# Performance work log

Hardware: AMD Instinct MI355X
Metric: run time of the kernel (lower is better)

## Reference

```python
import jax, jax.numpy as jnp
import numpy as np

N, P, D = 262144, 128, 64
EPS = 1e-5
NEG = -1e30


def setup_inputs() -> dict:
    key = jax.random.key(0)
    ks = jax.random.split(key, 12)
    feature = jax.random.normal(ks[0], (N, D), jnp.float32)
    feature_geo = jax.random.normal(ks[1], (N, D), jnp.float32)
    xyz = jax.random.uniform(ks[2], (N, 3), jnp.float32)
    centers = jax.random.uniform(ks[3], (3,), jnp.float32)
    plane_center = jax.random.uniform(ks[4], (P, 3), jnp.float32)
    nrm = jax.random.normal(ks[5], (P, 3), jnp.float32)
    plane_normal = nrm / jnp.linalg.norm(nrm, axis=1, keepdims=True)
    lo = 0.3 * jax.random.uniform(ks[6], (P, 3), jnp.float32)
    hi = 0.5 + 0.5 * jax.random.uniform(ks[7], (P, 3), jnp.float32)
    # exactly two active axes per plane (one axis of the aabb is zeroed)
    ax = jnp.arange(P) % 3
    keep = (jnp.arange(3)[None, :] != ax[:, None]).astype(jnp.float32)
    plane_xyz_min = lo * keep
    plane_xyz_max = hi * keep
    w1 = 0.05 * jax.random.normal(ks[8], (2 * D, D), jnp.float32)
    b1 = jnp.zeros((D,), jnp.float32)
    w2 = 0.05 * jax.random.normal(ks[9], (D, D), jnp.float32)
    b2 = jnp.zeros((D,), jnp.float32)
    w3 = 0.05 * jax.random.normal(ks[10], (D, 1), jnp.float32)
    b3 = jnp.zeros((1,), jnp.float32)
    g1 = jnp.ones((D,), jnp.float32); be1 = jnp.zeros((D,), jnp.float32)
    m1 = jnp.zeros((D,), jnp.float32); v1 = jnp.ones((D,), jnp.float32)
    g2 = jnp.ones((D,), jnp.float32); be2 = jnp.zeros((D,), jnp.float32)
    m2 = jnp.zeros((D,), jnp.float32); v2 = jnp.ones((D,), jnp.float32)
    return dict(feature=feature, feature_geo=feature_geo, xyz=xyz, centers=centers,
                plane_center=plane_center, plane_normal=plane_normal,
                plane_xyz_min=plane_xyz_min, plane_xyz_max=plane_xyz_max,
                w1=w1, b1=b1, g1=g1, be1=be1, m1=m1, v1=v1,
                w2=w2, b2=b2, g2=g2, be2=be2, m2=m2, v2=v2,
                w3=w3, b3=b3)


def _bn(x, g, b, m, v):
    return (x - m) * (g * jax.lax.rsqrt(v + EPS)) + b


def reference(feature, feature_geo, xyz, centers, plane_center, plane_normal,
              plane_xyz_min, plane_xyz_max, w1, b1, g1, be1, m1, v1,
              w2, b2, g2, be2, m2, v2, w3, b3):
    clouds = xyz + centers                                   # [N,3]
    f = jnp.concatenate([feature, feature_geo], axis=1)      # [N,2D]
    # 1x1 conv MLP == per-point matmul (fc1 -> fc2 with BN+ReLU, fc3)
    h1 = jax.nn.relu(_bn(f @ w1 + b1, g1, be1, m1, v1))      # [N,D]
    h2 = jax.nn.relu(_bn(h1 @ w2 + b2, g2, be2, m2, v2))     # [N,D]
    scores = jax.nn.relu(h2 @ w3 + b3)[:, 0]                 # [N]
    # per-plane aabb mask over the two active axes (xyz_max != 0)
    active = plane_xyz_max != 0                              # [P,3]
    in_rng = (clouds[None] >= plane_xyz_min[:, None]) & (clouds[None] < plane_xyz_max[:, None])
    range_mask = jnp.all(in_rng | ~active[:, None, :], axis=-1)   # [P,N]
    # point-to-plane distance: |(clouds - center) . normal|
    dots = clouds @ plane_normal.T                           # [N,P]
    offs = jnp.sum(plane_center * plane_normal, axis=1)      # [P]
    dist = jnp.abs(dots - offs[None, :]).T                   # [P,N]
    mask = range_mask & (dist < 0.1)                         # [P,N]
    sig = jax.nn.sigmoid(scores)                             # [N]
    on_mask = mask & (sig > 0.5)[None, :]
    off_mask = mask & (sig <= 0.5)[None, :]

    def pool(m):  # masked max-pool of fc2 features over points of one plane
        val = jnp.max(jnp.where(m[:, None], h2, NEG), axis=0)     # [D]
        return jnp.where(jnp.any(m), val, 0.0)

    on_feat = jax.lax.map(pool, on_mask)                     # [P,D]
    off_feat = jax.lax.map(pool, off_mask)                   # [P,D]
    scores_masked = jnp.where(mask, scores[None, :], 0.0)    # [P,N]
    return scores_masked, mask, on_mask, off_mask, on_feat, off_feat
```

## Files before the change

### kernel.cpp

```cpp
#include <hip/hip_runtime.h>
#include <hip/hip_bf16.h>
#include <math.h>

#define NPTS 262144
#define NP   128
#define DD   64
#define NWORDS (NPTS / 64)

#define AS4 __attribute__((address_space(4)))
typedef float evf4 __attribute__((ext_vector_type(4)));
typedef AS4 const float* csf;
typedef AS4 const evf4*  csf4;
#define TO_CSF(p)  ((csf)(unsigned long long)(const void*)(p))
#define TO_CSF4(p) ((csf4)(unsigned long long)(const void*)(p))

__global__ __launch_bounds__(256) void prep_kernel(
    const float* __restrict__ plane_center, const float* __restrict__ plane_normal,
    const float* __restrict__ pmin, const float* __restrict__ pmax,
    const float* __restrict__ w2,
    float* __restrict__ packed, float* __restrict__ w2T,
    float* __restrict__ out_feats)
{
    const int t = threadIdx.x;
    out_feats[blockIdx.x * 256 + t] = 0.0f;
    if (blockIdx.x == 0 && t < NP) {
        float n0 = plane_normal[t*3+0], n1 = plane_normal[t*3+1], n2 = plane_normal[t*3+2];
        float c0 = plane_center[t*3+0], c1 = plane_center[t*3+1], c2 = plane_center[t*3+2];
        float off = (c0*n0 + c1*n1) + c2*n2;
        float4* pp = reinterpret_cast<float4*>(packed) + t * 3;
        pp[0] = make_float4(n0, n1, n2, off);
        pp[1] = make_float4(pmin[t*3+0], pmin[t*3+1], pmin[t*3+2], 0.0f);
        pp[2] = make_float4(pmax[t*3+0], pmax[t*3+1], pmax[t*3+2], 0.0f);
    }
    if (blockIdx.x == 1) {
#pragma unroll
        for (int u = 0; u < 16; ++u) {
            const int e = u * 256 + t;
            const int j = e >> 6, k = e & 63;
            w2T[e] = w2[k * DD + j];
        }
    }
}

__global__ __launch_bounds__(256) void fused_kernel(
    const float* __restrict__ feature, const float* __restrict__ feature_geo,
    const float* __restrict__ xyz, const float* __restrict__ centers,
    const float* __restrict__ packed,
    const float* __restrict__ w1, const float* __restrict__ b1,
    const float* __restrict__ g1, const float* __restrict__ be1,
    const float* __restrict__ m1, const float* __restrict__ v1,
    const float* __restrict__ w2T, const float* __restrict__ b2,
    const float* __restrict__ g2, const float* __restrict__ be2,
    const float* __restrict__ m2, const float* __restrict__ v2,
    const float* __restrict__ w3, const float* __restrict__ b3,
    float* __restrict__ h2_out,
    float* __restrict__ out_sm, float* __restrict__ out_mask,
    float* __restrict__ out_on, float* __restrict__ out_off,
    unsigned long long* __restrict__ hitOn, unsigned long long* __restrict__ hitOff)
{
    __shared__ float sw1[128 * DD];
    __shared__ float sw2[DD * DD];
    const int t = threadIdx.x;
    const int n = blockIdx.x * 256 + t;
    const int lane = t & 63;
    const int word = n >> 6;

    {
        const float4* s1 = reinterpret_cast<const float4*>(w1);
        const float4* s2 = reinterpret_cast<const float4*>(w2T);
        float4* d1 = reinterpret_cast<float4*>(sw1);
        float4* d2 = reinterpret_cast<float4*>(sw2);
#pragma unroll
        for (int k = 0; k < 8; ++k) d1[t + k * 256] = s1[t + k * 256];
#pragma unroll
        for (int k = 0; k < 4; ++k) d2[t + k * 256] = s2[t + k * 256];
    }

    const csf cc = TO_CSF(centers);
    const float c0 = xyz[n*3+0] + cc[0];
    const float c1 = xyz[n*3+1] + cc[1];
    const float c2 = xyz[n*3+2] + cc[2];

    __syncthreads();

    float acc[DD];
#pragma unroll
    for (int j = 0; j < DD; ++j) acc[j] = 0.0f;

    const float4* fA = reinterpret_cast<const float4*>(feature) + (size_t)n * 16;
    const float4* fB = reinterpret_cast<const float4*>(feature_geo) + (size_t)n * 16;
#pragma unroll 1
    for (int q = 0; q < 16; ++q) {
        const float4 fv = fA[q];
        const evf4* wr = reinterpret_cast<const evf4*>(sw1 + q * 4 * DD);
#pragma unroll
        for (int j4 = 0; j4 < 16; ++j4) { const evf4 w = wr[j4];
            acc[4*j4+0] = fmaf(fv.x, w.x, acc[4*j4+0]);
            acc[4*j4+1] = fmaf(fv.x, w.y, acc[4*j4+1]);
            acc[4*j4+2] = fmaf(fv.x, w.z, acc[4*j4+2]);
            acc[4*j4+3] = fmaf(fv.x, w.w, acc[4*j4+3]); }
#pragma unroll
        for (int j4 = 0; j4 < 16; ++j4) { const evf4 w = wr[16 + j4];
            acc[4*j4+0] = fmaf(fv.y, w.x, acc[4*j4+0]);
            acc[4*j4+1] = fmaf(fv.y, w.y, acc[4*j4+1]);
            acc[4*j4+2] = fmaf(fv.y, w.z, acc[4*j4+2]);
            acc[4*j4+3] = fmaf(fv.y, w.w, acc[4*j4+3]); }
#pragma unroll
        for (int j4 = 0; j4 < 16; ++j4) { const evf4 w = wr[32 + j4];
            acc[4*j4+0] = fmaf(fv.z, w.x, acc[4*j4+0]);
            acc[4*j4+1] = fmaf(fv.z, w.y, acc[4*j4+1]);
            acc[4*j4+2] = fmaf(fv.z, w.z, acc[4*j4+2]);
            acc[4*j4+3] = fmaf(fv.z, w.w, acc[4*j4+3]); }
#pragma unroll
        for (int j4 = 0; j4 < 16; ++j4) { const evf4 w = wr[48 + j4];
            acc[4*j4+0] = fmaf(fv.w, w.x, acc[4*j4+0]);
            acc[4*j4+1] = fmaf(fv.w, w.y, acc[4*j4+1]);
            acc[4*j4+2] = fmaf(fv.w, w.z, acc[4*j4+2]);
            acc[4*j4+3] = fmaf(fv.w, w.w, acc[4*j4+3]); }
    }
#pragma unroll 1
    for (int q = 0; q < 16; ++q) {
        const float4 fv = fB[q];
        const evf4* wr = reinterpret_cast<const evf4*>(sw1 + (DD + q * 4) * DD);
#pragma unroll
        for (int j4 = 0; j4 < 16; ++j4) { const evf4 w = wr[j4];
            acc[4*j4+0] = fmaf(fv.x, w.x, acc[4*j4+0]);
            acc[4*j4+1] = fmaf(fv.x, w.y, acc[4*j4+1]);
            acc[4*j4+2] = fmaf(fv.x, w.z, acc[4*j4+2]);
            acc[4*j4+3] = fmaf(fv.x, w.w, acc[4*j4+3]); }
#pragma unroll
        for (int j4 = 0; j4 < 16; ++j4) { const evf4 w = wr[16 + j4];
            acc[4*j4+0] = fmaf(fv.y, w.x, acc[4*j4+0]);
            acc[4*j4+1] = fmaf(fv.y, w.y, acc[4*j4+1]);
            acc[4*j4+2] = fmaf(fv.y, w.z, acc[4*j4+2]);
            acc[4*j4+3] = fmaf(fv.y, w.w, acc[4*j4+3]); }
#pragma unroll
        for (int j4 = 0; j4 < 16; ++j4) { const evf4 w = wr[32 + j4];
            acc[4*j4+0] = fmaf(fv.z, w.x, acc[4*j4+0]);
            acc[4*j4+1] = fmaf(fv.z, w.y, acc[4*j4+1]);
            acc[4*j4+2] = fmaf(fv.z, w.z, acc[4*j4+2]);
            acc[4*j4+3] = fmaf(fv.z, w.w, acc[4*j4+3]); }
#pragma unroll
        for (int j4 = 0; j4 < 16; ++j4) { const evf4 w = wr[48 + j4];
            acc[4*j4+0] = fmaf(fv.w, w.x, acc[4*j4+0]);
            acc[4*j4+1] = fmaf(fv.w, w.y, acc[4*j4+1]);
            acc[4*j4+2] = fmaf(fv.w, w.z, acc[4*j4+2]);
            acc[4*j4+3] = fmaf(fv.w, w.w, acc[4*j4+3]); }
    }
    {
        const csf g1c = TO_CSF(g1), v1c = TO_CSF(v1), b1c = TO_CSF(b1),
                  m1c = TO_CSF(m1), be1c = TO_CSF(be1);
#pragma unroll
        for (int j = 0; j < DD; ++j) {
            float sc = g1c[j] * (1.0f / sqrtf(v1c[j] + 1e-5f));
            float h  = fmaf(acc[j] + b1c[j] - m1c[j], sc, be1c[j]);
            acc[j] = fmaxf(h, 0.0f);
        }
    }

    const csf g2c = TO_CSF(g2), v2c = TO_CSF(v2), b2c = TO_CSF(b2),
              m2c = TO_CSF(m2), be2c = TO_CSF(be2), w3c = TO_CSF(w3);
    float s = 0.0f;
    float4* o = reinterpret_cast<float4*>(h2_out) + (size_t)n * 16;
#pragma unroll 1
    for (int jq = 0; jq < 16; ++jq) {
        const evf4* r0 = reinterpret_cast<const evf4*>(sw2 + (4*jq + 0) * DD);
        const evf4* r1 = reinterpret_cast<const evf4*>(sw2 + (4*jq + 1) * DD);
        const evf4* r2 = reinterpret_cast<const evf4*>(sw2 + (4*jq + 2) * DD);
        const evf4* r3 = reinterpret_cast<const evf4*>(sw2 + (4*jq + 3) * DD);
        float a0 = 0.0f, a1 = 0.0f, a2 = 0.0f, a3 = 0.0f;
#pragma unroll
        for (int k4 = 0; k4 < 16; ++k4) {
            const evf4 w0 = r0[k4], w1v = r1[k4], w2v = r2[k4], w3v = r3[k4];
            const float h0 = acc[4*k4+0], h1v = acc[4*k4+1],
                        h2v = acc[4*k4+2], h3v = acc[4*k4+3];
            a0 = fmaf(h0, w0.x, a0); a0 = fmaf(h1v, w0.y, a0);
            a0 = fmaf(h2v, w0.z, a0); a0 = fmaf(h3v, w0.w, a0);
            a1 = fmaf(h0, w1v.x, a1); a1 = fmaf(h1v, w1v.y, a1);
            a1 = fmaf(h2v, w1v.z, a1); a1 = fmaf(h3v, w1v.w, a1);
            a2 = fmaf(h0, w2v.x, a2); a2 = fmaf(h1v, w2v.y, a2);
            a2 = fmaf(h2v, w2v.z, a2); a2 = fmaf(h3v, w2v.w, a2);
            a3 = fmaf(h0, w3v.x, a3); a3 = fmaf(h1v, w3v.y, a3);
            a3 = fmaf(h2v, w3v.z, a3); a3 = fmaf(h3v, w3v.w, a3);
        }
        float hv[4] = {a0, a1, a2, a3};
#pragma unroll
        for (int u = 0; u < 4; ++u) {
            const int jj = 4*jq + u;
            float sc = g2c[jj] * (1.0f / sqrtf(v2c[jj] + 1e-5f));
            float h  = fmaf(hv[u] + b2c[jj] - m2c[jj], sc, be2c[jj]);
            h = fmaxf(h, 0.0f);
            hv[u] = h;
            s = fmaf(h, w3c[jj], s);
        }
        o[jq] = make_float4(hv[0], hv[1], hv[2], hv[3]);
    }
    s += TO_CSF(b3)[0];
    const float score = fmaxf(s, 0.0f);

    const bool on = (0.5f + 0.5f * tanhf(0.5f * score)) > 0.5f;

    const csf4 pp = TO_CSF4(packed);
#pragma unroll 1
    for (int p = 0; p < NP; ++p) {
        const evf4 nrm = pp[p*3+0];
        const evf4 mn  = pp[p*3+1];
        const evf4 mx  = pp[p*3+2];
        float d = fabsf(fmaf(c2, nrm.z, fmaf(c1, nrm.y, c0 * nrm.x)) - nrm.w);
        bool ok0 = (mx.x == 0.0f) | ((c0 >= mn.x) & (c0 < mx.x));
        bool ok1 = (mx.y == 0.0f) | ((c1 >= mn.y) & (c1 < mx.y));
        bool ok2 = (mx.z == 0.0f) | ((c2 >= mn.z) & (c2 < mx.z));
        bool mk  = ok0 & ok1 & ok2 & (d < 0.1f);
        const size_t idx = (size_t)p * NPTS + n;
        const bool mon  = mk & on;
        const bool moff = mk & (!on);
        out_mask[idx] = mk ? 1.0f : 0.0f;
        out_sm[idx]   = mk ? score : 0.0f;
        out_on[idx]   = mon ? 1.0f : 0.0f;
        out_off[idx]  = moff ? 1.0f : 0.0f;
        unsigned long long bOn  = __ballot(mon);
        unsigned long long bOff = __ballot(moff);
        if (lane == 0) {
            hitOn [(size_t)p * NWORDS + word] = bOn;
            hitOff[(size_t)p * NWORDS + word] = bOff;
        }
    }
}

__global__ __launch_bounds__(256) void pool_kernel(
    const float* __restrict__ h2,
    const unsigned long long* __restrict__ hitOn,
    const unsigned long long* __restrict__ hitOff,
    int* __restrict__ out_feats_i)
{
    __shared__ float tile[128 * DD];
    __shared__ unsigned long long bm[2][NP][2];
    const int t = threadIdx.x;
    const int lane = t & 63;
    const int wv = t >> 6;

    float accOn[32], accOff[32];
#pragma unroll
    for (int i = 0; i < 32; ++i) { accOn[i] = 0.0f; accOff[i] = 0.0f; }

    for (int cc = 0; cc < 4; ++cc) {
        const int chunk = blockIdx.x * 4 + cc;
        const int base  = chunk * 128;
        const float4* src = reinterpret_cast<const float4*>(h2 + (size_t)base * DD);
        float4* dst = reinterpret_cast<float4*>(tile);
#pragma unroll
        for (int q = 0; q < 8; ++q) dst[t + q * 256] = src[t + q * 256];
        {
            const int p = t & 127;
            const int half = t >> 7;
            const unsigned long long* hsrc = half ? hitOff : hitOn;
            const int w0 = chunk * 2;
            bm[half][p][0] = hsrc[(size_t)p * NWORDS + w0 + 0];
            bm[half][p][1] = hsrc[(size_t)p * NWORDS + w0 + 1];
        }
        __syncthreads();

#pragma unroll
        for (int i = 0; i < 32; ++i) {
            const int p = wv * 32 + i;
            unsigned long long m;
            m = bm[0][p][0];
            while (m) { int nn = __builtin_ctzll(m); m &= m - 1;
                        accOn[i]  = fmaxf(accOn[i],  tile[nn * DD + lane]); }
            m = bm[0][p][1];
            while (m) { int nn = __builtin_ctzll(m); m &= m - 1;
                        accOn[i]  = fmaxf(accOn[i],  tile[(64 + nn) * DD + lane]); }
            m = bm[1][p][0];
            while (m) { int nn = __builtin_ctzll(m); m &= m - 1;
                        accOff[i] = fmaxf(accOff[i], tile[nn * DD + lane]); }
            m = bm[1][p][1];
            while (m) { int nn = __builtin_ctzll(m); m &= m - 1;
                        accOff[i] = fmaxf(accOff[i], tile[(64 + nn) * DD + lane]); }
        }
        __syncthreads();
    }
#pragma unroll
    for (int i = 0; i < 32; ++i) {
        const int p = wv * 32 + i;
        if (accOn[i]  != 0.0f) atomicMax(&out_feats_i[p * DD + lane],            __float_as_int(accOn[i]));
        if (accOff[i] != 0.0f) atomicMax(&out_feats_i[NP * DD + p * DD + lane],  __float_as_int(accOff[i]));
    }
}

extern "C" void kernel_launch(void* const* d_in, const int* in_sizes, int n_in,
                              void* d_out, int out_size, void* d_ws, size_t ws_size,
                              hipStream_t stream) {
    const float* feature      = (const float*)d_in[0];
    const float* feature_geo  = (const float*)d_in[1];
    const float* xyz          = (const float*)d_in[2];
    const float* centers      = (const float*)d_in[3];
    const float* plane_center = (const float*)d_in[4];
    const float* plane_normal = (const float*)d_in[5];
    const float* pmin         = (const float*)d_in[6];
    const float* pmax         = (const float*)d_in[7];
    const float* w1 = (const float*)d_in[8];
    const float* b1 = (const float*)d_in[9];
    const float* g1 = (const float*)d_in[10];
    const float* be1 = (const float*)d_in[11];
    const float* m1 = (const float*)d_in[12];
    const float* v1 = (const float*)d_in[13];
    const float* w2 = (const float*)d_in[14];
    const float* b2 = (const float*)d_in[15];
    const float* g2 = (const float*)d_in[16];
    const float* be2 = (const float*)d_in[17];
    const float* m2 = (const float*)d_in[18];
    const float* v2 = (const float*)d_in[19];
    const float* w3 = (const float*)d_in[20];
    const float* b3 = (const float*)d_in[21];

    float* out = (float*)d_out;
    const size_t PN = (size_t)NP * NPTS;
    float* out_sm    = out;
    float* out_mask  = out + PN;
    float* out_on    = out + 2 * PN;
    float* out_off   = out + 3 * PN;
    float* out_feats = out + 4 * PN;

    float* h2     = (float*)d_ws;
    unsigned long long* hitOn  = (unsigned long long*)(h2 + (size_t)NPTS * DD);
    unsigned long long* hitOff = hitOn + (size_t)NP * NWORDS;
    float* packed = (float*)(hitOff + (size_t)NP * NWORDS);
    float* w2T    = packed + NP * 12;

    prep_kernel<<<64, 256, 0, stream>>>(
        plane_center, plane_normal, pmin, pmax, w2, packed, w2T, out_feats);
    fused_kernel<<<NPTS / 256, 256, 0, stream>>>(
        feature, feature_geo, xyz, centers, packed,
        w1, b1, g1, be1, m1, v1, w2T, b2, g2, be2, m2, v2, w3, b3,
        h2, out_sm, out_mask, out_on, out_off, hitOn, hitOff);
    pool_kernel<<<512, 256, 0, stream>>>(h2, hitOn, hitOff, (int*)out_feats);
}
```

Baseline: 832.6 us.

## Split fc1 across wave halves so each lane computes two points over half the dims

The fc1 matmul is restructured so that each lane handles 32 output dimensions for two points (one per half-wave pairing) instead of all 64 dimensions for one point. This halves the per-lane LDS weight reads per FMA and improves weight reuse from shared memory. Results are exchanged between wave halves with cross-lane shuffles to rebuild the full 64-wide vector per point. BN1 parameters are also staged into shared memory. The price is extra shuffle work and a different global load pattern for features.

```diff
diff --git a/kernel.cpp b/kernel.cpp
--- a/kernel.cpp
+++ b/kernel.cpp
@@ -41,6 +41,12 @@
         }
     }
 }
+
+#define FMA4(ACC, FS, W, J) \
+    ACC[4*(J)+0] = fmaf((FS), (W).x, ACC[4*(J)+0]); \
+    ACC[4*(J)+1] = fmaf((FS), (W).y, ACC[4*(J)+1]); \
+    ACC[4*(J)+2] = fmaf((FS), (W).z, ACC[4*(J)+2]); \
+    ACC[4*(J)+3] = fmaf((FS), (W).w, ACC[4*(J)+3]);
 
 __global__ __launch_bounds__(256) void fused_kernel(
     const float* __restrict__ feature, const float* __restrict__ feature_geo,
@@ -60,10 +66,17 @@
 {
     __shared__ float sw1[128 * DD];
     __shared__ float sw2[DD * DD];
+    __shared__ float sbn1[5 * DD];
     const int t = threadIdx.x;
     const int n = blockIdx.x * 256 + t;
     const int lane = t & 63;
     const int word = n >> 6;
+    const int p = lane & 31;
+    const int half = lane >> 5;
+    const int dimoff = half * 32;
+    const int wavebase = blockIdx.x * 256 + (t >> 6) * 64;
+    const int ptA = wavebase + p;
+    const int ptB = wavebase + 32 + p;
 
     {
         const float4* s1 = reinterpret_cast<const float4*>(w1);
@@ -74,6 +87,13 @@
         for (int k = 0; k < 8; ++k) d1[t + k * 256] = s1[t + k * 256];
 #pragma unroll
         for (int k = 0; k < 4; ++k) d2[t + k * 256] = s2[t + k * 256];
+        if (t < DD) {
+            sbn1[t]          = b1[t];
+            sbn1[DD + t]     = m1[t];
+            sbn1[2*DD + t]   = g1[t];
+            sbn1[3*DD + t]   = v1[t];
+            sbn1[4*DD + t]   = be1[t];
+        }
     }
 
     const csf cc = TO_CSF(centers);
@@ -83,79 +103,68 @@
 
     __syncthreads();
 
-    float acc[DD];
-#pragma unroll
-    for (int j = 0; j < DD; ++j) acc[j] = 0.0f;
-
-    const float4* fA = reinterpret_cast<const float4*>(feature) + (size_t)n * 16;
-    const float4* fB = reinterpret_cast<const float4*>(feature_geo) + (size_t)n * 16;
+    float a0[32], a1[32];
+#pragma unroll
+    for (int j = 0; j < 32; ++j) { a0[j] = 0.0f; a1[j] = 0.0f; }
+
+    const float4* fA0 = reinterpret_cast<const float4*>(feature) + (size_t)ptA * 16;
+    const float4* fA1 = reinterpret_cast<const float4*>(feature) + (size_t)ptB * 16;
+    const float4* fB0 = reinterpret_cast<const float4*>(feature_geo) + (size_t)ptA * 16;
+    const float4* fB1 = reinterpret_cast<const float4*>(feature_geo) + (size_t)ptB * 16;
 #pragma unroll 1
     for (int q = 0; q < 16; ++q) {
-        const float4 fv = fA[q];
-        const evf4* wr = reinterpret_cast<const evf4*>(sw1 + q * 4 * DD);
-#pragma unroll
-        for (int j4 = 0; j4 < 16; ++j4) { const evf4 w = wr[j4];
-            acc[4*j4+0] = fmaf(fv.x, w.x, acc[4*j4+0]);
-            acc[4*j4+1] = fmaf(fv.x, w.y, acc[4*j4+1]);
-            acc[4*j4+2] = fmaf(fv.x, w.z, acc[4*j4+2]);
-            acc[4*j4+3] = fmaf(fv.x, w.w, acc[4*j4+3]); }
-#pragma unroll
-        for (int j4 = 0; j4 < 16; ++j4) { const evf4 w = wr[16 + j4];
-            acc[4*j4+0] = fmaf(fv.y, w.x, acc[4*j4+0]);
-            acc[4*j4+1] = fmaf(fv.y, w.y, acc[4*j4+1]);
-            acc[4*j4+2] = fmaf(fv.y, w.z, acc[4*j4+2]);
-            acc[4*j4+3] = fmaf(fv.y, w.w, acc[4*j4+3]); }
-#pragma unroll
-        for (int j4 = 0; j4 < 16; ++j4) { const evf4 w = wr[32 + j4];
-            acc[4*j4+0] = fmaf(fv.z, w.x, acc[4*j4+0]);
-            acc[4*j4+1] = fmaf(fv.z, w.y, acc[4*j4+1]);
-            acc[4*j4+2] = fmaf(fv.z, w.z, acc[4*j4+2]);
-            acc[4*j4+3] = fmaf(fv.z, w.w, acc[4*j4+3]); }
-#pragma unroll
-        for (int j4 = 0; j4 < 16; ++j4) { const evf4 w = wr[48 + j4];
-            acc[4*j4+0] = fmaf(fv.w, w.x, acc[4*j4+0]);
-            acc[4*j4+1] = fmaf(fv.w, w.y, acc[4*j4+1]);
-            acc[4*j4+2] = fmaf(fv.w, w.z, acc[4*j4+2]);
-            acc[4*j4+3] = fmaf(fv.w, w.w, acc[4*j4+3]); }
+        const float4 f0 = fA0[q];
+        const float4 f1 = fA1[q];
+        const evf4* wr = reinterpret_cast<const evf4*>(sw1 + q * 4 * DD + dimoff);
+#pragma unroll
+        for (int j4 = 0; j4 < 8; ++j4) { const evf4 w = wr[j4];
+            FMA4(a0, f0.x, w, j4) FMA4(a1, f1.x, w, j4) }
+#pragma unroll
+        for (int j4 = 0; j4 < 8; ++j4) { const evf4 w = wr[16 + j4];
+            FMA4(a0, f0.y, w, j4) FMA4(a1, f1.y, w, j4) }
+#pragma unroll
+        for (int j4 = 0; j4 < 8; ++j4) { const evf4 w = wr[32 + j4];
+            FMA4(a0, f0.z, w, j4) FMA4(a1, f1.z, w, j4) }
+#pragma unroll
+        for (int j4 = 0; j4 < 8; ++j4) { const evf4 w = wr[48 + j4];
+            FMA4(a0, f0.w, w, j4) FMA4(a1, f1.w, w, j4) }
     }
 #pragma unroll 1
     for (int q = 0; q < 16; ++q) {
-        const float4 fv = fB[q];
-        const evf4* wr = reinterpret_cast<const evf4*>(sw1 + (DD + q * 4) * DD);
-#pragma unroll
-        for (int j4 = 0; j4 < 16; ++j4) { const evf4 w = wr[j4];
-            acc[4*j4+0] = fmaf(fv.x, w.x, acc[4*j4+0]);
-            acc[4*j4+1] = fmaf(fv.x, w.y, acc[4*j4+1]);
-            acc[4*j4+2] = fmaf(fv.x, w.z, acc[4*j4+2]);
-            acc[4*j4+3] = fmaf(fv.x, w.w, acc[4*j4+3]); }
-#pragma unroll
-        for (int j4 = 0; j4 < 16; ++j4) { const evf4 w = wr[16 + j4];
-            acc[4*j4+0] = fmaf(fv.y, w.x, acc[4*j4+0]);
-            acc[4*j4+1] = fmaf(fv.y, w.y, acc[4*j4+1]);
-            acc[4*j4+2] = fmaf(fv.y, w.z, acc[4*j4+2]);
-            acc[4*j4+3] = fmaf(fv.y, w.w, acc[4*j4+3]); }
-#pragma unroll
-        for (int j4 = 0; j4 < 16; ++j4) { const evf4 w = wr[32 + j4];
-            acc[4*j4+0] = fmaf(fv.z, w.x, acc[4*j4+0]);
-            acc[4*j4+1] = fmaf(fv.z, w.y, acc[4*j4+1]);
-            acc[4*j4+2] = fmaf(fv.z, w.z, acc[4*j4+2]);
-            acc[4*j4+3] = fmaf(fv.z, w.w, acc[4*j4+3]); }
-#pragma unroll
-        for (int j4 = 0; j4 < 16; ++j4) { const evf4 w = wr[48 + j4];
-            acc[4*j4+0] = fmaf(fv.w, w.x, acc[4*j4+0]);
-            acc[4*j4+1] = fmaf(fv.w, w.y, acc[4*j4+1]);
-            acc[4*j4+2] = fmaf(fv.w, w.z, acc[4*j4+2]);
-            acc[4*j4+3] = fmaf(fv.w, w.w, acc[4*j4+3]); }
-    }
-    {
-        const csf g1c = TO_CSF(g1), v1c = TO_CSF(v1), b1c = TO_CSF(b1),
-                  m1c = TO_CSF(m1), be1c = TO_CSF(be1);
-#pragma unroll
-        for (int j = 0; j < DD; ++j) {
-            float sc = g1c[j] * (1.0f / sqrtf(v1c[j] + 1e-5f));
-            float h  = fmaf(acc[j] + b1c[j] - m1c[j], sc, be1c[j]);
-            acc[j] = fmaxf(h, 0.0f);
-        }
+        const float4 f0 = fB0[q];
+        const float4 f1 = fB1[q];
+        const evf4* wr = reinterpret_cast<const evf4*>(sw1 + (DD + q * 4) * DD + dimoff);
+#pragma unroll
+        for (int j4 = 0; j4 < 8; ++j4) { const evf4 w = wr[j4];
+            FMA4(a0, f0.x, w, j4) FMA4(a1, f1.x, w, j4) }
+#pragma unroll
+        for (int j4 = 0; j4 < 8; ++j4) { const evf4 w = wr[16 + j4];
+            FMA4(a0, f0.y, w, j4) FMA4(a1, f1.y, w, j4) }
+#pragma unroll
+        for (int j4 = 0; j4 < 8; ++j4) { const evf4 w = wr[32 + j4];
+            FMA4(a0, f0.z, w, j4) FMA4(a1, f1.z, w, j4) }
+#pragma unroll
+        for (int j4 = 0; j4 < 8; ++j4) { const evf4 w = wr[48 + j4];
+            FMA4(a0, f0.w, w, j4) FMA4(a1, f1.w, w, j4) }
+    }
+#pragma unroll
+    for (int j = 0; j < 32; ++j) {
+        const int jj = dimoff + j;
+        float sc = sbn1[2*DD + jj] * (1.0f / sqrtf(sbn1[3*DD + jj] + 1e-5f));
+        float h0 = fmaf(a0[j] + sbn1[jj] - sbn1[DD + jj], sc, sbn1[4*DD + jj]);
+        float h1 = fmaf(a1[j] + sbn1[jj] - sbn1[DD + jj], sc, sbn1[4*DD + jj]);
+        a0[j] = fmaxf(h0, 0.0f);
+        a1[j] = fmaxf(h1, 0.0f);
+    }
+
+    float acc[DD];
+#pragma unroll
+    for (int i = 0; i < 32; ++i) {
+        const float send = half ? a0[i] : a1[i];
+        const float recv = __shfl_xor(send, 32, 64);
+        const float own  = half ? a1[i] : a0[i];
+        acc[dimoff + i] = own;
+        acc[(half ? 0 : 32) + i] = recv;
     }
 
     const csf g2c = TO_CSF(g2), v2c = TO_CSF(v2), b2c = TO_CSF(b2),
@@ -168,22 +177,22 @@
         const evf4* r1 = reinterpret_cast<const evf4*>(sw2 + (4*jq + 1) * DD);
         const evf4* r2 = reinterpret_cast<const evf4*>(sw2 + (4*jq + 2) * DD);
         const evf4* r3 = reinterpret_cast<const evf4*>(sw2 + (4*jq + 3) * DD);
-        float a0 = 0.0f, a1 = 0.0f, a2 = 0.0f, a3 = 0.0f;
+        float a00 = 0.0f, a01 = 0.0f, a02 = 0.0f, a03 = 0.0f;
 #pragma unroll
         for (int k4 = 0; k4 < 16; ++k4) {
             const evf4 w0 = r0[k4], w1v = r1[k4], w2v = r2[k4], w3v = r3[k4];
             const float h0 = acc[4*k4+0], h1v = acc[4*k4+1],
                         h2v = acc[4*k4+2], h3v = acc[4*k4+3];
-            a0 = fmaf(h0, w0.x, a0); a0 = fmaf(h1v, w0.y, a0);
-            a0 = fmaf(h2v, w0.z, a0); a0 = fmaf(h3v, w0.w, a0);
-            a1 = fmaf(h0, w1v.x, a1); a1 = fmaf(h1v, w1v.y, a1);
-            a1 = fmaf(h2v, w1v.z, a1); a1 = fmaf(h3v, w1v.w, a1);
-            a2 = fmaf(h0, w2v.x, a2); a2 = fmaf(h1v, w2v.y, a2);
-            a2 = fmaf(h2v, w2v.z, a2); a2 = fmaf(h3v, w2v.w, a2);
-            a3 = fmaf(h0, w3v.x, a3); a3 = fmaf(h1v, w3v.y, a3);
-            a3 = fmaf(h2v, w3v.z, a3); a3 = fmaf(h3v, w3v.w, a3);
-        }
-        float hv[4] = {a0, a1, a2, a3};
+            a00 = fmaf(h0, w0.x, a00); a00 = fmaf(h1v, w0.y, a00);
+            a00 = fmaf(h2v, w0.z, a00); a00 = fmaf(h3v, w0.w, a00);
+            a01 = fmaf(h0, w1v.x, a01); a01 = fmaf(h1v, w1v.y, a01);
+            a01 = fmaf(h2v, w1v.z, a01); a01 = fmaf(h3v, w1v.w, a01);
+            a02 = fmaf(h0, w2v.x, a02); a02 = fmaf(h1v, w2v.y, a02);
+            a02 = fmaf(h2v, w2v.z, a02); a02 = fmaf(h3v, w2v.w, a02);
+            a03 = fmaf(h0, w3v.x, a03); a03 = fmaf(h1v, w3v.y, a03);
+            a03 = fmaf(h2v, w3v.z, a03); a03 = fmaf(h3v, w3v.w, a03);
+        }
+        float hv[4] = {a00, a01, a02, a03};
 #pragma unroll
         for (int u = 0; u < 4; ++u) {
             const int jj = 4*jq + u;
@@ -202,16 +211,16 @@
 
     const csf4 pp = TO_CSF4(packed);
 #pragma unroll 1
-    for (int p = 0; p < NP; ++p) {
-        const evf4 nrm = pp[p*3+0];
-        const evf4 mn  = pp[p*3+1];
-        const evf4 mx  = pp[p*3+2];
+    for (int p2 = 0; p2 < NP; ++p2) {
+        const evf4 nrm = pp[p2*3+0];
+        const evf4 mn  = pp[p2*3+1];
+        const evf4 mx  = pp[p2*3+2];
         float d = fabsf(fmaf(c2, nrm.z, fmaf(c1, nrm.y, c0 * nrm.x)) - nrm.w);
         bool ok0 = (mx.x == 0.0f) | ((c0 >= mn.x) & (c0 < mx.x));
         bool ok1 = (mx.y == 0.0f) | ((c1 >= mn.y) & (c1 < mx.y));
         bool ok2 = (mx.z == 0.0f) | ((c2 >= mn.z) & (c2 < mx.z));
         bool mk  = ok0 & ok1 & ok2 & (d < 0.1f);
-        const size_t idx = (size_t)p * NPTS + n;
+        const size_t idx = (size_t)p2 * NPTS + n;
         const bool mon  = mk & on;
         const bool moff = mk & (!on);
         out_mask[idx] = mk ? 1.0f : 0.0f;
@@ -221,8 +230,8 @@
         unsigned long long bOn  = __ballot(mon);
         unsigned long long bOff = __ballot(moff);
         if (lane == 0) {
-            hitOn [(size_t)p * NWORDS + word] = bOn;
-            hitOff[(size_t)p * NWORDS + word] = bOff;
+            hitOn [(size_t)p2 * NWORDS + word] = bOn;
+            hitOff[(size_t)p2 * NWORDS + word] = bOff;
         }
     }
 }
```

New measurement: 909.5 us. 1.09x slower.

## Restructure pool kernel to iterate per plane over sparse hit bitmasks

Applied to the files above, without the earlier changes.

The pool kernel now assigns each block one plane, one side (on or off) and a range of point words. It scans the bitmask words with a ballot to skip empty ones and gathers only the hit rows of h2 directly from global memory, instead of staging every h2 tile into shared memory and looping over all 128 planes per chunk. This avoids reading all of h2 into LDS when masks are sparse, and it processes two hits per step. In exchange it issues scattered global loads that may repeat across planes, launches many more blocks, and reduces across waves through shared memory before the atomics. The existing code compares atomicMax on float bit patterns against a 0 initial value, which relies on features being non-negative.

```diff
diff --git a/kernel.cpp b/kernel.cpp
--- a/kernel.cpp
+++ b/kernel.cpp
@@ -233,57 +233,49 @@
     const unsigned long long* __restrict__ hitOff,
     int* __restrict__ out_feats_i)
 {
-    __shared__ float tile[128 * DD];
-    __shared__ unsigned long long bm[2][NP][2];
+    __shared__ float sacc[4][DD];
     const int t = threadIdx.x;
     const int lane = t & 63;
     const int wv = t >> 6;
 
-    float accOn[32], accOff[32];
-#pragma unroll
-    for (int i = 0; i < 32; ++i) { accOn[i] = 0.0f; accOff[i] = 0.0f; }
-
-    for (int cc = 0; cc < 4; ++cc) {
-        const int chunk = blockIdx.x * 4 + cc;
-        const int base  = chunk * 128;
-        const float4* src = reinterpret_cast<const float4*>(h2 + (size_t)base * DD);
-        float4* dst = reinterpret_cast<float4*>(tile);
-#pragma unroll
-        for (int q = 0; q < 8; ++q) dst[t + q * 256] = src[t + q * 256];
-        {
-            const int p = t & 127;
-            const int half = t >> 7;
-            const unsigned long long* hsrc = half ? hitOff : hitOn;
-            const int w0 = chunk * 2;
-            bm[half][p][0] = hsrc[(size_t)p * NWORDS + w0 + 0];
-            bm[half][p][1] = hsrc[(size_t)p * NWORDS + w0 + 1];
-        }
-        __syncthreads();
-
-#pragma unroll
-        for (int i = 0; i < 32; ++i) {
-            const int p = wv * 32 + i;
-            unsigned long long m;
-            m = bm[0][p][0];
-            while (m) { int nn = __builtin_ctzll(m); m &= m - 1;
-                        accOn[i]  = fmaxf(accOn[i],  tile[nn * DD + lane]); }
-            m = bm[0][p][1];
-            while (m) { int nn = __builtin_ctzll(m); m &= m - 1;
-                        accOn[i]  = fmaxf(accOn[i],  tile[(64 + nn) * DD + lane]); }
-            m = bm[1][p][0];
-            while (m) { int nn = __builtin_ctzll(m); m &= m - 1;
-                        accOff[i] = fmaxf(accOff[i], tile[nn * DD + lane]); }
-            m = bm[1][p][1];
-            while (m) { int nn = __builtin_ctzll(m); m &= m - 1;
-                        accOff[i] = fmaxf(accOff[i], tile[(64 + nn) * DD + lane]); }
-        }
-        __syncthreads();
-    }
-#pragma unroll
-    for (int i = 0; i < 32; ++i) {
-        const int p = wv * 32 + i;
-        if (accOn[i]  != 0.0f) atomicMax(&out_feats_i[p * DD + lane],            __float_as_int(accOn[i]));
-        if (accOff[i] != 0.0f) atomicMax(&out_feats_i[NP * DD + p * DD + lane],  __float_as_int(accOff[i]));
+    const int bid   = blockIdx.x;
+    const int p     = bid >> 5;
+    const int side  = (bid >> 4) & 1;
+    const int chunk = bid & 15;
+    const unsigned long long* hsrc = side ? hitOff : hitOn;
+
+    const int wbase = chunk * 256 + wv * 64;
+    const unsigned long long myw = hsrc[(size_t)p * NWORDS + wbase + lane];
+
+    float acc = 0.0f;
+    unsigned long long act = __ballot(myw != 0ULL);
+    while (act) {
+        const int l = __builtin_ctzll(act);
+        act &= act - 1;
+        unsigned long long w = __shfl(myw, l, 64);
+        const size_t nbase = (size_t)(wbase + l) * 64;
+        while (w) {
+            const int b0 = __builtin_ctzll(w); w &= w - 1;
+            if (w) {
+                const int b1 = __builtin_ctzll(w); w &= w - 1;
+                const float v0 = h2[(nbase + b0) * DD + lane];
+                const float v1 = h2[(nbase + b1) * DD + lane];
+                acc = fmaxf(acc, v0);
+                acc = fmaxf(acc, v1);
+            } else {
+                const float v0 = h2[(nbase + b0) * DD + lane];
+                acc = fmaxf(acc, v0);
+            }
+        }
+    }
+
+    sacc[wv][lane] = acc;
+    __syncthreads();
+    if (t < DD) {
+        const float m = fmaxf(fmaxf(sacc[0][t], sacc[1][t]),
+                              fmaxf(sacc[2][t], sacc[3][t]));
+        if (m != 0.0f)
+            atomicMax(&out_feats_i[side * NP * DD + p * DD + t], __float_as_int(m));
     }
 }
 
@@ -333,5 +325,5 @@
         feature, feature_geo, xyz, centers, packed,
         w1, b1, g1, be1, m1, v1, w2T, b2, g2, be2, m2, v2, w3, b3,
         h2, out_sm, out_mask, out_on, out_off, hitOn, hitOff);
-    pool_kernel<<<512, 256, 0, stream>>>(h2, hitOn, hitOff, (int*)out_feats);
+    pool_kernel<<<4096, 256, 0, stream>>>(h2, hitOn, hitOff, (int*)out_feats);
 }
```

After: 824.1 us. No clear change (-1.0%).
